# Optimization experiments

Hardware: AMD Instinct MI355X
Metric: run time of the kernel (lower is better)

Reference implementation:

```python
import jax, jax.numpy as jnp
import numpy as np

B, S, D = 4, 2048, 2048  # batch, seq, input_dim == state_dim
N = D

def setup_inputs() -> dict:
    key = jax.random.key(0)
    ks = jax.random.split(key, 6)
    x = jax.random.normal(ks[0], (B, S, D), dtype=jnp.float32)
    W_dt = jax.random.normal(ks[1], (N, D), dtype=jnp.float32) / np.sqrt(D)
    b_dt = jnp.ones((N,), dtype=jnp.float32)  # dt_proj.bias.fill_(1.0)
    W_B = jax.random.normal(ks[2], (N, D), dtype=jnp.float32) / np.sqrt(D)
    W_C = jax.random.normal(ks[3], (D, N), dtype=jnp.float32) / np.sqrt(N)
    A_log = jax.random.normal(ks[4], (N,), dtype=jnp.float32) * 0.5 - 1.0
    D_skip = jnp.zeros((D,), dtype=jnp.float32)
    return {"x": x, "W_dt": W_dt, "b_dt": b_dt, "W_B": W_B, "W_C": W_C,
            "A_log": A_log, "D_skip": D_skip}

def reference(x, W_dt, b_dt, W_B, W_C, A_log, D_skip):
    # dt = softplus(x @ W_dt^T + b_dt) -> [B,S,N]
    dt = jax.nn.softplus(jnp.einsum('bsd,nd->bsn', x, W_dt) + b_dt)
    Bp = jnp.einsum('bsd,nd->bsn', x, W_B)          # [B,S,N]
    A = -jnp.exp(A_log)                              # [N]
    A_bar = jnp.exp(dt * A)                          # [B,S,N]
    inputs = (dt * Bp) * x                           # B_bar * x (N == D)
    # selective scan: h_t = A_bar_t * h_{t-1} + inputs_t
    h0 = jnp.zeros((x.shape[0], A_log.shape[0]), dtype=x.dtype)
    def step(h, ab_u):
        ab, u = ab_u
        h = ab * h + u
        return h, h
    # scan over time axis: move S to leading axis
    _, h_all = jax.lax.scan(step, h0,
                            (jnp.swapaxes(A_bar, 0, 1), jnp.swapaxes(inputs, 0, 1)))
    h_all = jnp.swapaxes(h_all, 0, 1)                # [B,S,N]
    out = jnp.einsum('bsn,dn->bsd', h_all, W_C) + D_skip * x
    return out
```

## Files before the change

### kernel.cpp

```cpp
#include <hip/hip_runtime.h>

#define SEQ    2048
#define DIM    2048
#define NBATCH 4
#define MTOT   (NBATCH * SEQ)
#define CHUNKS 32
#define CLEN   (SEQ / CHUNKS)
#define HT_ELEMS (256 * 32)

typedef __bf16 bf16_t;
typedef __bf16 bf16x8 __attribute__((ext_vector_type(8)));
typedef float  f32x4  __attribute__((ext_vector_type(4)));
typedef unsigned short u16x4 __attribute__((ext_vector_type(4)));
typedef unsigned short u16x2 __attribute__((ext_vector_type(2)));

typedef __attribute__((address_space(3))) bf16_t lds_bf16;

__device__ __forceinline__ unsigned short f2bf_rne(float f) {
    unsigned int u = __float_as_uint(f);
    u += 0x7fffu + ((u >> 16) & 1u);
    return (unsigned short)(u >> 16);
}
__device__ __forceinline__ float bf2f(unsigned short v) {
    return __uint_as_float((unsigned int)v << 16);
}

__global__ void k_convert(const float* __restrict__ src,
                          unsigned short* __restrict__ dst, int n4) {
    int i = blockIdx.x * blockDim.x + threadIdx.x;
    if (i >= n4) return;
    f32x4 v = ((const f32x4*)src)[i];
    u16x4 o;
    o[0] = f2bf_rne(v[0]); o[1] = f2bf_rne(v[1]);
    o[2] = f2bf_rne(v[2]); o[3] = f2bf_rne(v[3]);
    ((u16x4*)dst)[i] = o;
}

__global__ void k_convert_ilv(const float* __restrict__ src,
                              unsigned short* __restrict__ dst, int n4, int phase) {
    int i = blockIdx.x * blockDim.x + threadIdx.x;
    if (i >= n4) return;
    const int R4 = DIM / 4;
    int nrow = i / R4;
    int dcol = i - nrow * R4;
    f32x4 v = ((const f32x4*)src)[i];
    u16x4 o;
    o[0] = f2bf_rne(v[0]); o[1] = f2bf_rne(v[1]);
    o[2] = f2bf_rne(v[2]); o[3] = f2bf_rne(v[3]);
    ((u16x4*)dst)[(2 * nrow + phase) * R4 + dcol] = o;
}

__global__ void k_prep_a(const float* __restrict__ A_log, float* __restrict__ negA, int n) {
    int i = blockIdx.x * blockDim.x + threadIdx.x;
    if (i < n) negA[i] = -__expf(A_log[i]);
}

__device__ __forceinline__ void stage_half(const bf16_t* __restrict__ g, long rowbase,
                                           int K, int k0, bf16_t* lds,
                                           int wave, int lane) {
    const int rl     = lane >> 2;
    const int gchunk = (lane & 3) ^ ((lane >> 3) & 3);
#pragma unroll
    for (int q = 0; q < 2; q++) {
        const bf16_t* ga = g + (rowbase + wave * 32 + q * 16 + rl) * (long)K
                             + k0 + gchunk * 8;
        __builtin_amdgcn_global_load_lds(
            (const __attribute__((address_space(1))) void*)ga,
            (__attribute__((address_space(3))) void*)((char*)lds + (wave * 32 + q * 16) * 64),
            16, 0, 0);
    }
}

#define MFMA_B16(a, b, c) __builtin_amdgcn_mfma_f32_16x16x32_bf16(a, b, c, 0, 0, 0)
#define BAR  __builtin_amdgcn_s_barrier()
#define SBAR __builtin_amdgcn_sched_barrier(0)
#define DSR(D, P) asm volatile("ds_read_b128 %0, %1" : "=v"(D) : "v"(P))

template <int KTILES>
__device__ __forceinline__ void gemm256_main(const bf16_t* __restrict__ A,
                                             const bf16_t* __restrict__ Bm,
                                             int K, long arow0, long brow0,
                                             bf16_t* As, bf16_t* Bs,
                                             f32x4 acc[8][4],
                                             int wave, int lane, int wm, int wn) {
    const int l15  = lane & 15;
    const int quad = lane >> 4;
    const int swz  = (quad ^ ((l15 >> 1) & 3)) * 8;
    const int aoff = (wm * 128 + l15) * 32 + swz;
    const int boff = (wn * 64  + l15) * 32 + swz;

    const lds_bf16* Aw = ((const lds_bf16*)As) + aoff;
    const lds_bf16* Bw = ((const lds_bf16*)Bs) + boff;

    auto stA = [&](int buf, int ks, int kt) {
        stage_half(A, arow0, K, kt * 64 + ks * 32, As + (buf * 2 + ks) * HT_ELEMS, wave, lane);
    };
    auto stB = [&](int buf, int ks, int kt) {
        stage_half(Bm, brow0, K, kt * 64 + ks * 32, Bs + (buf * 2 + ks) * HT_ELEMS, wave, lane);
    };

    stB(0, 0, 0); stA(0, 0, 0); stB(0, 1, 0); stA(0, 1, 0);
    stB(1, 0, 1); stA(1, 0, 1); stB(1, 1, 1);
    asm volatile("s_waitcnt vmcnt(6)");
    SBAR;
    BAR;

    bf16x8 a0, a1, a2, a3, b0, b1, b2, b3;

#define LDA03(BUF, KS) { const lds_bf16* p = Aw + ((BUF) * 2 + (KS)) * HT_ELEMS; \
    DSR(a0, p); DSR(a1, p + 512); DSR(a2, p + 1024); DSR(a3, p + 1536); }
#define LDA47(BUF, KS) { const lds_bf16* p = Aw + ((BUF) * 2 + (KS)) * HT_ELEMS + 2048; \
    DSR(a0, p); DSR(a1, p + 512); DSR(a2, p + 1024); DSR(a3, p + 1536); }
#define LDB(BUF, KS)  { const lds_bf16* p = Bw + ((BUF) * 2 + (KS)) * HT_ELEMS; \
    DSR(b0, p); DSR(b1, p + 512); DSR(b2, p + 1024); DSR(b3, p + 1536); }
#define MM16(I0) \
    SBAR; \
    BAR; \
    asm volatile("s_waitcnt lgkmcnt(0)"); \
    SBAR; \
    __builtin_amdgcn_s_setprio(1); \
    acc[(I0)+0][0] = MFMA_B16(a0, b0, acc[(I0)+0][0]); \
    acc[(I0)+0][1] = MFMA_B16(a0, b1, acc[(I0)+0][1]); \
    acc[(I0)+0][2] = MFMA_B16(a0, b2, acc[(I0)+0][2]); \
    acc[(I0)+0][3] = MFMA_B16(a0, b3, acc[(I0)+0][3]); \
    acc[(I0)+1][0] = MFMA_B16(a1, b0, acc[(I0)+1][0]); \
    acc[(I0)+1][1] = MFMA_B16(a1, b1, acc[(I0)+1][1]); \
    acc[(I0)+1][2] = MFMA_B16(a1, b2, acc[(I0)+1][2]); \
    acc[(I0)+1][3] = MFMA_B16(a1, b3, acc[(I0)+1][3]); \
    acc[(I0)+2][0] = MFMA_B16(a2, b0, acc[(I0)+2][0]); \
    acc[(I0)+2][1] = MFMA_B16(a2, b1, acc[(I0)+2][1]); \
    acc[(I0)+2][2] = MFMA_B16(a2, b2, acc[(I0)+2][2]); \
    acc[(I0)+2][3] = MFMA_B16(a2, b3, acc[(I0)+2][3]); \
    acc[(I0)+3][0] = MFMA_B16(a3, b0, acc[(I0)+3][0]); \
    acc[(I0)+3][1] = MFMA_B16(a3, b1, acc[(I0)+3][1]); \
    acc[(I0)+3][2] = MFMA_B16(a3, b2, acc[(I0)+3][2]); \
    acc[(I0)+3][3] = MFMA_B16(a3, b3, acc[(I0)+3][3]); \
    __builtin_amdgcn_s_setprio(0); \
    SBAR; \
    BAR;

#pragma unroll 1
    for (int t = 0; t < KTILES / 2; ++t) {
        const bool nlast = (t != KTILES / 2 - 1);
        const int k1 = 2 * t + 1, k2 = 2 * t + 2, k3 = 2 * t + 3;
        LDA03(0, 0); LDB(0, 0);
        stA(1, 1, k1);
        MM16(0);
        LDA47(0, 0);
        if (nlast) stB(0, 0, k2);
        MM16(4);
        LDA03(0, 1); LDB(0, 1);
        if (nlast) stA(0, 0, k2);
        MM16(0);
        LDA47(0, 1);
        if (nlast) stB(0, 1, k2);
        if (nlast) { asm volatile("s_waitcnt vmcnt(6)"); }
        else       { asm volatile("s_waitcnt vmcnt(0)"); }
        MM16(4);
        LDA03(1, 0); LDB(1, 0);
        if (nlast) stA(0, 1, k2);
        MM16(0);
        LDA47(1, 0);
        if (nlast) stB(1, 0, k3);
        MM16(4);
        LDA03(1, 1); LDB(1, 1);
        if (nlast) stA(1, 0, k3);
        MM16(0);
        LDA47(1, 1);
        if (nlast) stB(1, 1, k3);
        if (nlast) { asm volatile("s_waitcnt vmcnt(6)"); }
        MM16(4);
    }
#undef LDA03
#undef LDA47
#undef LDB
#undef MM16
}

__global__ __launch_bounds__(512, 2)
void k_gemm_fused(const bf16_t* __restrict__ A, const bf16_t* __restrict__ Wcat,
                  const float* __restrict__ x, const float* __restrict__ b_dt,
                  const float* __restrict__ negA,
                  unsigned short* __restrict__ abuf, unsigned short* __restrict__ ubuf) {
    __shared__ __align__(16) bf16_t As[4 * HT_ELEMS];
    __shared__ __align__(16) bf16_t Bs[4 * HT_ELEMS];

    const int tid  = threadIdx.x;
    const int lane = tid & 63;
    const int wave = tid >> 6;
    const int wm   = wave >> 2;
    const int wn   = wave & 3;
    int flat = blockIdx.x;
    int swzb = (flat & 7) * 64 + (flat >> 3);
    int bm = swzb & 31;
    int bn = swzb >> 5;

    f32x4 acc[8][4];
#pragma unroll
    for (int i = 0; i < 8; i++)
#pragma unroll
        for (int j = 0; j < 4; j++) acc[i][j] = (f32x4){0.f, 0.f, 0.f, 0.f};

    gemm256_main<DIM / 64>(A, Wcat, DIM, (long)bm * 256, (long)bn * 256,
                           As, Bs, acc, wave, lane, wm, wn);

    const int l15  = lane & 15;
    const int quad = lane >> 4;
    const int odd  = l15 & 1;
#pragma unroll
    for (int i = 0; i < 8; i++) {
#pragma unroll
        for (int j = 0; j < 4; j++) {
#pragma unroll
            for (int r = 0; r < 4; r++) {
                float v = acc[i][j][r];
                float w = __shfl_xor(v, 1);
                float dtpre = odd ? w : v;
                float bpv   = odd ? v : w;
                long row = (long)bm * 256 + wm * 128 + i * 16 + quad * 4 + r;
                int  col = bn * 256 + wn * 64 + j * 16 + l15;
                int  n   = col >> 1;
                float z  = dtpre + b_dt[n];
                float dt = (z > 15.f) ? z : __logf(1.f + __expf(z));
                float a  = __expf(negA[n] * dt);
                float u  = dt * bpv * x[row * DIM + n];
                long idx = row * DIM + n;
                if (odd) ubuf[idx] = f2bf_rne(u); else abuf[idx] = f2bf_rne(a);
            }
        }
    }
}

__global__ __launch_bounds__(512, 2)
void k_gemm_bt(const bf16_t* __restrict__ A, const bf16_t* __restrict__ Bm,
               float* __restrict__ C, int N, int K,
               const float* __restrict__ skip, const float* __restrict__ xres) {
    __shared__ __align__(16) bf16_t As[4 * HT_ELEMS];
    __shared__ __align__(16) bf16_t Bs[4 * HT_ELEMS];

    const int tid  = threadIdx.x;
    const int lane = tid & 63;
    const int wave = tid >> 6;
    const int wm   = wave >> 2;
    const int wn   = wave & 3;
    int flat = blockIdx.x;
    int swzb = (flat & 7) * 32 + (flat >> 3);
    int bm = swzb & 31;
    int bn = swzb >> 5;

    f32x4 acc[8][4];
#pragma unroll
    for (int i = 0; i < 8; i++)
#pragma unroll
        for (int j = 0; j < 4; j++) acc[i][j] = (f32x4){0.f, 0.f, 0.f, 0.f};

    gemm256_main<DIM / 64>(A, Bm, K, (long)bm * 256, (long)bn * 256,
                           As, Bs, acc, wave, lane, wm, wn);

    const int l15  = lane & 15;
    const int quad = lane >> 4;
#pragma unroll
    for (int i = 0; i < 8; i++) {
#pragma unroll
        for (int j = 0; j < 4; j++) {
#pragma unroll
            for (int r = 0; r < 4; r++) {
                long row = (long)bm * 256 + wm * 128 + i * 16 + quad * 4 + r;
                long col = (long)bn * 256 + wn * 64 + j * 16 + l15;
                long idx = row * (long)N + col;
                float v = acc[i][j][r];
                if (skip) v += skip[col] * xres[idx];
                C[idx] = v;
            }
        }
    }
}

__global__ void k_scan1(const unsigned short* __restrict__ a,
                        const unsigned short* __restrict__ u,
                        float* __restrict__ P, float* __restrict__ V) {
    int t  = blockIdx.x * blockDim.x + threadIdx.x;
    int n2 = t & (DIM / 2 - 1);
    int c  = (t >> 10) & (CHUNKS - 1);
    int b  = t >> 15;
    long base = ((long)b * SEQ + (long)c * CLEN) * DIM + n2 * 2;
    float p0 = 1.f, v0 = 0.f, p1 = 1.f, v1 = 0.f;
    for (int s = 0; s < CLEN; s++) {
        u16x2 av = *(const u16x2*)(a + base + (long)s * DIM);
        u16x2 uv = *(const u16x2*)(u + base + (long)s * DIM);
        float a0 = bf2f(av[0]), a1 = bf2f(av[1]);
        v0 = a0 * v0 + bf2f(uv[0]);  p0 *= a0;
        v1 = a1 * v1 + bf2f(uv[1]);  p1 *= a1;
    }
    long pidx = ((long)b * CHUNKS + c) * DIM + n2 * 2;
    *(float2*)(P + pidx) = make_float2(p0, p1);
    *(float2*)(V + pidx) = make_float2(v0, v1);
}

__global__ void k_scan2(const float* __restrict__ P, const float* __restrict__ V,
                        float* __restrict__ carry) {
    int t = blockIdx.x * blockDim.x + threadIdx.x;
    int n = t & (DIM - 1);
    int b = t >> 11;
    float H = 0.f;
    for (int c = 0; c < CHUNKS; c++) {
        long idx = ((long)b * CHUNKS + c) * DIM + n;
        carry[idx] = H;
        H = P[idx] * H + V[idx];
    }
}

__global__ void k_scan3(const unsigned short* __restrict__ a,
                        const unsigned short* __restrict__ u,
                        const float* __restrict__ carry,
                        unsigned short* __restrict__ h) {
    int t  = blockIdx.x * blockDim.x + threadIdx.x;
    int n2 = t & (DIM / 2 - 1);
    int c  = (t >> 10) & (CHUNKS - 1);
    int b  = t >> 15;
    long base = ((long)b * SEQ + (long)c * CLEN) * DIM + n2 * 2;
    long cidx = ((long)b * CHUNKS + c) * DIM + n2 * 2;
    float2 Hc = *(const float2*)(carry + cidx);
    float H0 = Hc.x, H1 = Hc.y;
    for (int s = 0; s < CLEN; s++) {
        u16x2 av = *(const u16x2*)(a + base + (long)s * DIM);
        u16x2 uv = *(const u16x2*)(u + base + (long)s * DIM);
        H0 = bf2f(av[0]) * H0 + bf2f(uv[0]);
        H1 = bf2f(av[1]) * H1 + bf2f(uv[1]);
        u16x2 o; o[0] = f2bf_rne(H0); o[1] = f2bf_rne(H1);
        *(u16x2*)(h + base + (long)s * DIM) = o;
    }
}

extern "C" void kernel_launch(void* const* d_in, const int* in_sizes, int n_in,
                              void* d_out, int out_size, void* d_ws, size_t ws_size,
                              hipStream_t stream) {
    const float* x      = (const float*)d_in[0];
    const float* W_dt   = (const float*)d_in[1];
    const float* b_dt   = (const float*)d_in[2];
    const float* W_B    = (const float*)d_in[3];
    const float* W_C    = (const float*)d_in[4];
    const float* A_log  = (const float*)d_in[5];
    const float* D_skip = (const float*)d_in[6];
    float* out = (float*)d_out;

    char* ws = (char*)d_ws;
    size_t off = 0;
    auto alloc = [&](size_t bytes) -> char* {
        char* p = ws + off;
        off += (bytes + 255) & ~(size_t)255;
        return p;
    };
    unsigned short* xb   = (unsigned short*)alloc((size_t)MTOT * DIM * 2);
    unsigned short* wcat = (unsigned short*)alloc((size_t)2 * DIM * DIM * 2);
    unsigned short* wcb  = (unsigned short*)alloc((size_t)DIM * DIM * 2);
    unsigned short* abuf = (unsigned short*)alloc((size_t)MTOT * DIM * 2);
    unsigned short* ubuf = (unsigned short*)alloc((size_t)MTOT * DIM * 2);
    float* P     = (float*)alloc((size_t)NBATCH * CHUNKS * DIM * 4);
    float* V     = (float*)alloc((size_t)NBATCH * CHUNKS * DIM * 4);
    float* carry = (float*)alloc((size_t)NBATCH * CHUNKS * DIM * 4);
    float* negA  = (float*)alloc((size_t)DIM * 4);

    const int n4x = MTOT * DIM / 4;
    const int n4w = DIM * DIM / 4;
    k_convert<<<n4x / 256, 256, 0, stream>>>(x, xb, n4x);
    k_convert_ilv<<<n4w / 256, 256, 0, stream>>>(W_dt, wcat, n4w, 0);
    k_convert_ilv<<<n4w / 256, 256, 0, stream>>>(W_B,  wcat, n4w, 1);
    k_convert<<<n4w / 256, 256, 0, stream>>>(W_C, wcb, n4w);
    k_prep_a<<<DIM / 256, 256, 0, stream>>>(A_log, negA, DIM);

    k_gemm_fused<<<(MTOT / 256) * (2 * DIM / 256), 512, 0, stream>>>(
        (const bf16_t*)xb, (const bf16_t*)wcat, x, b_dt, negA, abuf, ubuf);

    const int scan2_threads = NBATCH * CHUNKS * DIM / 2;
    k_scan1<<<scan2_threads / 256, 256, 0, stream>>>(abuf, ubuf, P, V);
    k_scan2<<<(NBATCH * DIM) / 256, 256, 0, stream>>>(P, V, carry);
    k_scan3<<<scan2_threads / 256, 256, 0, stream>>>(abuf, ubuf, carry, xb );

    k_gemm_bt<<<(MTOT / 256) * (DIM / 256), 512, 0, stream>>>(
        (const bf16_t*)xb, (const bf16_t*)wcb, out, DIM, DIM, D_skip, x);
}
```

Before: 501.0 us.

## Use partial LDS waits in GEMM inner loop and raise scan chunk count

The GEMM inner loop now interleaves the A and B LDS reads and swaps the single full lgkmcnt(0) wait for staged partial waits, reordering the MFMAs so each one starts as soon as its operands arrive. This is meant to overlap LDS read latency with matrix-core work. Separately, the chunked scan goes from 32 to 128 chunks, giving scan1 and scan3 four times as many threads with shorter sequential loops for more parallelism. The cost is a longer serial loop in scan2 and larger P/V/carry buffers.

```diff
diff --git a/kernel.cpp b/kernel.cpp
--- a/kernel.cpp
+++ b/kernel.cpp
@@ -4,8 +4,9 @@
 #define DIM    2048
 #define NBATCH 4
 #define MTOT   (NBATCH * SEQ)
-#define CHUNKS 32
+#define CHUNKS 128
 #define CLEN   (SEQ / CHUNKS)
+#define CSH    7
 #define HT_ELEMS (256 * 32)
 
 typedef __bf16 bf16_t;
@@ -75,6 +76,8 @@
 #define BAR  __builtin_amdgcn_s_barrier()
 #define SBAR __builtin_amdgcn_sched_barrier(0)
 #define DSR(D, P) asm volatile("ds_read_b128 %0, %1" : "=v"(D) : "v"(P))
+#define WAITL(N) do { asm volatile("s_waitcnt lgkmcnt(" #N ")"); \
+                      __builtin_amdgcn_sched_barrier(0); } while (0)
 
 template <int KTILES>
 __device__ __forceinline__ void gemm256_main(const bf16_t* __restrict__ A,
@@ -107,74 +110,105 @@
 
     bf16x8 a0, a1, a2, a3, b0, b1, b2, b3;
 
-#define LDA03(BUF, KS) { const lds_bf16* p = Aw + ((BUF) * 2 + (KS)) * HT_ELEMS; \
-    DSR(a0, p); DSR(a1, p + 512); DSR(a2, p + 1024); DSR(a3, p + 1536); }
-#define LDA47(BUF, KS) { const lds_bf16* p = Aw + ((BUF) * 2 + (KS)) * HT_ELEMS + 2048; \
-    DSR(a0, p); DSR(a1, p + 512); DSR(a2, p + 1024); DSR(a3, p + 1536); }
-#define LDB(BUF, KS)  { const lds_bf16* p = Bw + ((BUF) * 2 + (KS)) * HT_ELEMS; \
-    DSR(b0, p); DSR(b1, p + 512); DSR(b2, p + 1024); DSR(b3, p + 1536); }
-#define MM16(I0) \
-    SBAR; \
-    BAR; \
-    asm volatile("s_waitcnt lgkmcnt(0)"); \
-    SBAR; \
+#define LDAB03(BUF, KS) { \
+    const lds_bf16* pa = Aw + ((BUF) * 2 + (KS)) * HT_ELEMS; \
+    const lds_bf16* pb = Bw + ((BUF) * 2 + (KS)) * HT_ELEMS; \
+    DSR(a0, pa);        DSR(b0, pb); \
+    DSR(a1, pa + 512);  DSR(b1, pb + 512); \
+    DSR(a2, pa + 1024); DSR(b2, pb + 1024); \
+    DSR(a3, pa + 1536); DSR(b3, pb + 1536); }
+#define LDA47(BUF, KS) { \
+    const lds_bf16* pa = Aw + ((BUF) * 2 + (KS)) * HT_ELEMS + 2048; \
+    DSR(a0, pa); DSR(a1, pa + 512); DSR(a2, pa + 1024); DSR(a3, pa + 1536); }
+
+#define MM16A(I0) \
+    SBAR; BAR; \
+    WAITL(6); \
     __builtin_amdgcn_s_setprio(1); \
     acc[(I0)+0][0] = MFMA_B16(a0, b0, acc[(I0)+0][0]); \
+    WAITL(4); \
     acc[(I0)+0][1] = MFMA_B16(a0, b1, acc[(I0)+0][1]); \
-    acc[(I0)+0][2] = MFMA_B16(a0, b2, acc[(I0)+0][2]); \
-    acc[(I0)+0][3] = MFMA_B16(a0, b3, acc[(I0)+0][3]); \
     acc[(I0)+1][0] = MFMA_B16(a1, b0, acc[(I0)+1][0]); \
     acc[(I0)+1][1] = MFMA_B16(a1, b1, acc[(I0)+1][1]); \
+    WAITL(2); \
+    acc[(I0)+0][2] = MFMA_B16(a0, b2, acc[(I0)+0][2]); \
     acc[(I0)+1][2] = MFMA_B16(a1, b2, acc[(I0)+1][2]); \
-    acc[(I0)+1][3] = MFMA_B16(a1, b3, acc[(I0)+1][3]); \
     acc[(I0)+2][0] = MFMA_B16(a2, b0, acc[(I0)+2][0]); \
     acc[(I0)+2][1] = MFMA_B16(a2, b1, acc[(I0)+2][1]); \
     acc[(I0)+2][2] = MFMA_B16(a2, b2, acc[(I0)+2][2]); \
+    WAITL(0); \
+    acc[(I0)+0][3] = MFMA_B16(a0, b3, acc[(I0)+0][3]); \
+    acc[(I0)+1][3] = MFMA_B16(a1, b3, acc[(I0)+1][3]); \
     acc[(I0)+2][3] = MFMA_B16(a2, b3, acc[(I0)+2][3]); \
     acc[(I0)+3][0] = MFMA_B16(a3, b0, acc[(I0)+3][0]); \
     acc[(I0)+3][1] = MFMA_B16(a3, b1, acc[(I0)+3][1]); \
     acc[(I0)+3][2] = MFMA_B16(a3, b2, acc[(I0)+3][2]); \
     acc[(I0)+3][3] = MFMA_B16(a3, b3, acc[(I0)+3][3]); \
     __builtin_amdgcn_s_setprio(0); \
-    SBAR; \
-    BAR;
+    SBAR; BAR;
+
+#define MM16B(I0) \
+    SBAR; BAR; \
+    WAITL(3); \
+    __builtin_amdgcn_s_setprio(1); \
+    acc[(I0)+0][0] = MFMA_B16(a0, b0, acc[(I0)+0][0]); \
+    acc[(I0)+0][1] = MFMA_B16(a0, b1, acc[(I0)+0][1]); \
+    acc[(I0)+0][2] = MFMA_B16(a0, b2, acc[(I0)+0][2]); \
+    acc[(I0)+0][3] = MFMA_B16(a0, b3, acc[(I0)+0][3]); \
+    WAITL(2); \
+    acc[(I0)+1][0] = MFMA_B16(a1, b0, acc[(I0)+1][0]); \
+    acc[(I0)+1][1] = MFMA_B16(a1, b1, acc[(I0)+1][1]); \
+    acc[(I0)+1][2] = MFMA_B16(a1, b2, acc[(I0)+1][2]); \
+    acc[(I0)+1][3] = MFMA_B16(a1, b3, acc[(I0)+1][3]); \
+    WAITL(1); \
+    acc[(I0)+2][0] = MFMA_B16(a2, b0, acc[(I0)+2][0]); \
+    acc[(I0)+2][1] = MFMA_B16(a2, b1, acc[(I0)+2][1]); \
+    acc[(I0)+2][2] = MFMA_B16(a2, b2, acc[(I0)+2][2]); \
+    acc[(I0)+2][3] = MFMA_B16(a2, b3, acc[(I0)+2][3]); \
+    WAITL(0); \
+    acc[(I0)+3][0] = MFMA_B16(a3, b0, acc[(I0)+3][0]); \
+    acc[(I0)+3][1] = MFMA_B16(a3, b1, acc[(I0)+3][1]); \
+    acc[(I0)+3][2] = MFMA_B16(a3, b2, acc[(I0)+3][2]); \
+    acc[(I0)+3][3] = MFMA_B16(a3, b3, acc[(I0)+3][3]); \
+    __builtin_amdgcn_s_setprio(0); \
+    SBAR; BAR;
 
 #pragma unroll 1
     for (int t = 0; t < KTILES / 2; ++t) {
         const bool nlast = (t != KTILES / 2 - 1);
         const int k1 = 2 * t + 1, k2 = 2 * t + 2, k3 = 2 * t + 3;
-        LDA03(0, 0); LDB(0, 0);
+        LDAB03(0, 0);
         stA(1, 1, k1);
-        MM16(0);
+        MM16A(0);
         LDA47(0, 0);
         if (nlast) stB(0, 0, k2);
-        MM16(4);
-        LDA03(0, 1); LDB(0, 1);
+        MM16B(4);
+        LDAB03(0, 1);
         if (nlast) stA(0, 0, k2);
-        MM16(0);
+        MM16A(0);
         LDA47(0, 1);
         if (nlast) stB(0, 1, k2);
         if (nlast) { asm volatile("s_waitcnt vmcnt(6)"); }
         else       { asm volatile("s_waitcnt vmcnt(0)"); }
-        MM16(4);
-        LDA03(1, 0); LDB(1, 0);
+        MM16B(4);
+        LDAB03(1, 0);
         if (nlast) stA(0, 1, k2);
-        MM16(0);
+        MM16A(0);
         LDA47(1, 0);
         if (nlast) stB(1, 0, k3);
-        MM16(4);
-        LDA03(1, 1); LDB(1, 1);
+        MM16B(4);
+        LDAB03(1, 1);
         if (nlast) stA(1, 0, k3);
-        MM16(0);
+        MM16A(0);
         LDA47(1, 1);
         if (nlast) stB(1, 1, k3);
         if (nlast) { asm volatile("s_waitcnt vmcnt(6)"); }
-        MM16(4);
-    }
-#undef LDA03
+        MM16B(4);
+    }
+#undef LDAB03
 #undef LDA47
-#undef LDB
-#undef MM16
+#undef MM16A
+#undef MM16B
 }
 
 __global__ __launch_bounds__(512, 2)
@@ -282,7 +316,7 @@
     int t  = blockIdx.x * blockDim.x + threadIdx.x;
     int n2 = t & (DIM / 2 - 1);
     int c  = (t >> 10) & (CHUNKS - 1);
-    int b  = t >> 15;
+    int b  = t >> (10 + CSH);
     long base = ((long)b * SEQ + (long)c * CLEN) * DIM + n2 * 2;
     float p0 = 1.f, v0 = 0.f, p1 = 1.f, v1 = 0.f;
     for (int s = 0; s < CLEN; s++) {
@@ -317,7 +351,7 @@
     int t  = blockIdx.x * blockDim.x + threadIdx.x;
     int n2 = t & (DIM / 2 - 1);
     int c  = (t >> 10) & (CHUNKS - 1);
-    int b  = t >> 15;
+    int b  = t >> (10 + CSH);
     long base = ((long)b * SEQ + (long)c * CLEN) * DIM + n2 * 2;
     long cidx = ((long)b * CHUNKS + c) * DIM + n2 * 2;
     float2 Hc = *(const float2*)(carry + cidx);
@@ -372,10 +406,10 @@
     k_gemm_fused<<<(MTOT / 256) * (2 * DIM / 256), 512, 0, stream>>>(
         (const bf16_t*)xb, (const bf16_t*)wcat, x, b_dt, negA, abuf, ubuf);
 
-    const int scan2_threads = NBATCH * CHUNKS * DIM / 2;
-    k_scan1<<<scan2_threads / 256, 256, 0, stream>>>(abuf, ubuf, P, V);
+    const int scan_threads = NBATCH * CHUNKS * DIM / 2;
+    k_scan1<<<scan_threads / 256, 256, 0, stream>>>(abuf, ubuf, P, V);
     k_scan2<<<(NBATCH * DIM) / 256, 256, 0, stream>>>(P, V, carry);
-    k_scan3<<<scan2_threads / 256, 256, 0, stream>>>(abuf, ubuf, carry, xb );
+    k_scan3<<<scan_threads / 256, 256, 0, stream>>>(abuf, ubuf, carry, xb );
 
     k_gemm_bt<<<(MTOT / 256) * (DIM / 256), 512, 0, stream>>>(
         (const bf16_t*)xb, (const bf16_t*)wcb, out, DIM, DIM, D_skip, x);
```

Measured after the change: 509.9 us. Within noise of the previous version (+1.8%).

## Double-buffer LDS fragment registers to overlap ds_reads with MFMA phases

Applied to the files above, without the earlier changes.

Restructures the GEMM main loop so the LDS fragments for the next MFMA phase are read into a second register set while the current phase's MFMAs run. Each phase now has a single barrier instead of two. The prologue stages all eight tile halves, and vmcnt waits are adjusted to allow eight loads in flight. This costs more VGPRs for the extra fragment registers, which could pressure occupancy under launch_bounds(512,2). The CSH macro in the scan kernels is a cosmetic rename with the same shift value.

```diff
diff --git a/kernel.cpp b/kernel.cpp
--- a/kernel.cpp
+++ b/kernel.cpp
@@ -6,6 +6,7 @@
 #define MTOT   (NBATCH * SEQ)
 #define CHUNKS 32
 #define CLEN   (SEQ / CHUNKS)
+#define CSH    5
 #define HT_ELEMS (256 * 32)
 
 typedef __bf16 bf16_t;
@@ -75,6 +76,10 @@
 #define BAR  __builtin_amdgcn_s_barrier()
 #define SBAR __builtin_amdgcn_sched_barrier(0)
 #define DSR(D, P) asm volatile("ds_read_b128 %0, %1" : "=v"(D) : "v"(P))
+#define PRIO1 __builtin_amdgcn_s_setprio(1)
+#define PRIO0 __builtin_amdgcn_s_setprio(0)
+#define WAIT0 do { asm volatile("s_waitcnt lgkmcnt(0)"); SBAR; } while (0)
+#define ENDPH do { SBAR; BAR; } while (0)
 
 template <int KTILES>
 __device__ __forceinline__ void gemm256_main(const bf16_t* __restrict__ A,
@@ -99,81 +104,111 @@
         stage_half(Bm, brow0, K, kt * 64 + ks * 32, Bs + (buf * 2 + ks) * HT_ELEMS, wave, lane);
     };
 
+    bf16x8 aA0, aA1, aA2, aA3, aB0, aB1, aB2, aB3;
+    bf16x8 b00, b01, b02, b03, b10, b11, b12, b13;
+
+#define RD_FULL(BUF, KS, A0, A1, A2, A3, B0, B1, B2, B3) { \
+    const lds_bf16* pa = Aw + ((BUF) * 2 + (KS)) * HT_ELEMS; \
+    const lds_bf16* pb = Bw + ((BUF) * 2 + (KS)) * HT_ELEMS; \
+    DSR(A0, pa);        DSR(B0, pb); \
+    DSR(A1, pa + 512);  DSR(B1, pb + 512); \
+    DSR(A2, pa + 1024); DSR(B2, pb + 1024); \
+    DSR(A3, pa + 1536); DSR(B3, pb + 1536); }
+#define RD_HALF(BUF, KS, A0, A1, A2, A3) { \
+    const lds_bf16* pa = Aw + ((BUF) * 2 + (KS)) * HT_ELEMS + 2048; \
+    DSR(A0, pa); DSR(A1, pa + 512); DSR(A2, pa + 1024); DSR(A3, pa + 1536); }
+#define MM16(I0, A0, A1, A2, A3, B0, B1, B2, B3) do { \
+    PRIO1; \
+    acc[(I0)+0][0] = MFMA_B16(A0, B0, acc[(I0)+0][0]); \
+    acc[(I0)+0][1] = MFMA_B16(A0, B1, acc[(I0)+0][1]); \
+    acc[(I0)+0][2] = MFMA_B16(A0, B2, acc[(I0)+0][2]); \
+    acc[(I0)+0][3] = MFMA_B16(A0, B3, acc[(I0)+0][3]); \
+    acc[(I0)+1][0] = MFMA_B16(A1, B0, acc[(I0)+1][0]); \
+    acc[(I0)+1][1] = MFMA_B16(A1, B1, acc[(I0)+1][1]); \
+    acc[(I0)+1][2] = MFMA_B16(A1, B2, acc[(I0)+1][2]); \
+    acc[(I0)+1][3] = MFMA_B16(A1, B3, acc[(I0)+1][3]); \
+    acc[(I0)+2][0] = MFMA_B16(A2, B0, acc[(I0)+2][0]); \
+    acc[(I0)+2][1] = MFMA_B16(A2, B1, acc[(I0)+2][1]); \
+    acc[(I0)+2][2] = MFMA_B16(A2, B2, acc[(I0)+2][2]); \
+    acc[(I0)+2][3] = MFMA_B16(A2, B3, acc[(I0)+2][3]); \
+    acc[(I0)+3][0] = MFMA_B16(A3, B0, acc[(I0)+3][0]); \
+    acc[(I0)+3][1] = MFMA_B16(A3, B1, acc[(I0)+3][1]); \
+    acc[(I0)+3][2] = MFMA_B16(A3, B2, acc[(I0)+3][2]); \
+    acc[(I0)+3][3] = MFMA_B16(A3, B3, acc[(I0)+3][3]); \
+    PRIO0; } while (0)
+
     stB(0, 0, 0); stA(0, 0, 0); stB(0, 1, 0); stA(0, 1, 0);
-    stB(1, 0, 1); stA(1, 0, 1); stB(1, 1, 1);
-    asm volatile("s_waitcnt vmcnt(6)");
+    stB(1, 0, 1); stA(1, 0, 1); stB(1, 1, 1); stA(1, 1, 1);
+    asm volatile("s_waitcnt vmcnt(0)");
     SBAR;
     BAR;
-
-    bf16x8 a0, a1, a2, a3, b0, b1, b2, b3;
-
-#define LDA03(BUF, KS) { const lds_bf16* p = Aw + ((BUF) * 2 + (KS)) * HT_ELEMS; \
-    DSR(a0, p); DSR(a1, p + 512); DSR(a2, p + 1024); DSR(a3, p + 1536); }
-#define LDA47(BUF, KS) { const lds_bf16* p = Aw + ((BUF) * 2 + (KS)) * HT_ELEMS + 2048; \
-    DSR(a0, p); DSR(a1, p + 512); DSR(a2, p + 1024); DSR(a3, p + 1536); }
-#define LDB(BUF, KS)  { const lds_bf16* p = Bw + ((BUF) * 2 + (KS)) * HT_ELEMS; \
-    DSR(b0, p); DSR(b1, p + 512); DSR(b2, p + 1024); DSR(b3, p + 1536); }
-#define MM16(I0) \
-    SBAR; \
-    BAR; \
-    asm volatile("s_waitcnt lgkmcnt(0)"); \
-    SBAR; \
-    __builtin_amdgcn_s_setprio(1); \
-    acc[(I0)+0][0] = MFMA_B16(a0, b0, acc[(I0)+0][0]); \
-    acc[(I0)+0][1] = MFMA_B16(a0, b1, acc[(I0)+0][1]); \
-    acc[(I0)+0][2] = MFMA_B16(a0, b2, acc[(I0)+0][2]); \
-    acc[(I0)+0][3] = MFMA_B16(a0, b3, acc[(I0)+0][3]); \
-    acc[(I0)+1][0] = MFMA_B16(a1, b0, acc[(I0)+1][0]); \
-    acc[(I0)+1][1] = MFMA_B16(a1, b1, acc[(I0)+1][1]); \
-    acc[(I0)+1][2] = MFMA_B16(a1, b2, acc[(I0)+1][2]); \
-    acc[(I0)+1][3] = MFMA_B16(a1, b3, acc[(I0)+1][3]); \
-    acc[(I0)+2][0] = MFMA_B16(a2, b0, acc[(I0)+2][0]); \
-    acc[(I0)+2][1] = MFMA_B16(a2, b1, acc[(I0)+2][1]); \
-    acc[(I0)+2][2] = MFMA_B16(a2, b2, acc[(I0)+2][2]); \
-    acc[(I0)+2][3] = MFMA_B16(a2, b3, acc[(I0)+2][3]); \
-    acc[(I0)+3][0] = MFMA_B16(a3, b0, acc[(I0)+3][0]); \
-    acc[(I0)+3][1] = MFMA_B16(a3, b1, acc[(I0)+3][1]); \
-    acc[(I0)+3][2] = MFMA_B16(a3, b2, acc[(I0)+3][2]); \
-    acc[(I0)+3][3] = MFMA_B16(a3, b3, acc[(I0)+3][3]); \
-    __builtin_amdgcn_s_setprio(0); \
-    SBAR; \
-    BAR;
+    RD_FULL(0, 0, aA0, aA1, aA2, aA3, b00, b01, b02, b03);
 
 #pragma unroll 1
     for (int t = 0; t < KTILES / 2; ++t) {
         const bool nlast = (t != KTILES / 2 - 1);
         const int k1 = 2 * t + 1, k2 = 2 * t + 2, k3 = 2 * t + 3;
-        LDA03(0, 0); LDB(0, 0);
-        stA(1, 1, k1);
-        MM16(0);
-        LDA47(0, 0);
+
+        WAIT0;
+        RD_HALF(0, 0, aB0, aB1, aB2, aB3);
+        if (t) stA(1, 1, k1);
+        SBAR; asm volatile("s_waitcnt vmcnt(8)"); SBAR;
+        MM16(0, aA0, aA1, aA2, aA3, b00, b01, b02, b03);
+        ENDPH;
+        WAIT0;
+        RD_FULL(0, 1, aA0, aA1, aA2, aA3, b10, b11, b12, b13);
         if (nlast) stB(0, 0, k2);
-        MM16(4);
-        LDA03(0, 1); LDB(0, 1);
+        SBAR;
+        MM16(4, aB0, aB1, aB2, aB3, b00, b01, b02, b03);
+        ENDPH;
+        WAIT0;
+        RD_HALF(0, 1, aB0, aB1, aB2, aB3);
         if (nlast) stA(0, 0, k2);
-        MM16(0);
-        LDA47(0, 1);
+        SBAR;
+        if (nlast) { asm volatile("s_waitcnt vmcnt(8)"); }
+        else       { asm volatile("s_waitcnt vmcnt(4)"); }
+        SBAR;
+        MM16(0, aA0, aA1, aA2, aA3, b10, b11, b12, b13);
+        ENDPH;
+        WAIT0;
+        RD_FULL(1, 0, aA0, aA1, aA2, aA3, b00, b01, b02, b03);
         if (nlast) stB(0, 1, k2);
-        if (nlast) { asm volatile("s_waitcnt vmcnt(6)"); }
+        SBAR;
+        MM16(4, aB0, aB1, aB2, aB3, b10, b11, b12, b13);
+        ENDPH;
+        WAIT0;
+        RD_HALF(1, 0, aB0, aB1, aB2, aB3);
+        if (nlast) stA(0, 1, k2);
+        SBAR;
+        if (nlast) { asm volatile("s_waitcnt vmcnt(8)"); }
         else       { asm volatile("s_waitcnt vmcnt(0)"); }
-        MM16(4);
-        LDA03(1, 0); LDB(1, 0);
-        if (nlast) stA(0, 1, k2);
-        MM16(0);
-        LDA47(1, 0);
+        SBAR;
+        MM16(0, aA0, aA1, aA2, aA3, b00, b01, b02, b03);
+        ENDPH;
+        WAIT0;
+        RD_FULL(1, 1, aA0, aA1, aA2, aA3, b10, b11, b12, b13);
         if (nlast) stB(1, 0, k3);
-        MM16(4);
-        LDA03(1, 1); LDB(1, 1);
+        SBAR;
+        MM16(4, aB0, aB1, aB2, aB3, b00, b01, b02, b03);
+        ENDPH;
+        WAIT0;
+        RD_HALF(1, 1, aB0, aB1, aB2, aB3);
         if (nlast) stA(1, 0, k3);
-        MM16(0);
-        LDA47(1, 1);
-        if (nlast) stB(1, 1, k3);
-        if (nlast) { asm volatile("s_waitcnt vmcnt(6)"); }
-        MM16(4);
-    }
-#undef LDA03
-#undef LDA47
-#undef LDB
+        SBAR;
+        if (nlast) { asm volatile("s_waitcnt vmcnt(8)"); SBAR; }
+        MM16(0, aA0, aA1, aA2, aA3, b10, b11, b12, b13);
+        ENDPH;
+        WAIT0;
+        if (nlast) {
+            RD_FULL(0, 0, aA0, aA1, aA2, aA3, b00, b01, b02, b03);
+            stB(1, 1, k3);
+        }
+        SBAR;
+        MM16(4, aB0, aB1, aB2, aB3, b10, b11, b12, b13);
+        ENDPH;
+    }
+#undef RD_FULL
+#undef RD_HALF
 #undef MM16
 }
 
@@ -282,7 +317,7 @@
     int t  = blockIdx.x * blockDim.x + threadIdx.x;
     int n2 = t & (DIM / 2 - 1);
     int c  = (t >> 10) & (CHUNKS - 1);
-    int b  = t >> 15;
+    int b  = t >> (10 + CSH);
     long base = ((long)b * SEQ + (long)c * CLEN) * DIM + n2 * 2;
     float p0 = 1.f, v0 = 0.f, p1 = 1.f, v1 = 0.f;
     for (int s = 0; s < CLEN; s++) {
@@ -317,7 +352,7 @@
     int t  = blockIdx.x * blockDim.x + threadIdx.x;
     int n2 = t & (DIM / 2 - 1);
     int c  = (t >> 10) & (CHUNKS - 1);
-    int b  = t >> 15;
+    int b  = t >> (10 + CSH);
     long base = ((long)b * SEQ + (long)c * CLEN) * DIM + n2 * 2;
     long cidx = ((long)b * CHUNKS + c) * DIM + n2 * 2;
     float2 Hc = *(const float2*)(carry + cidx);
@@ -372,10 +407,10 @@
     k_gemm_fused<<<(MTOT / 256) * (2 * DIM / 256), 512, 0, stream>>>(
         (const bf16_t*)xb, (const bf16_t*)wcat, x, b_dt, negA, abuf, ubuf);
 
-    const int scan2_threads = NBATCH * CHUNKS * DIM / 2;
-    k_scan1<<<scan2_threads / 256, 256, 0, stream>>>(abuf, ubuf, P, V);
+    const int scan_threads = NBATCH * CHUNKS * DIM / 2;
+    k_scan1<<<scan_threads / 256, 256, 0, stream>>>(abuf, ubuf, P, V);
     k_scan2<<<(NBATCH * DIM) / 256, 256, 0, stream>>>(P, V, carry);
-    k_scan3<<<scan2_threads / 256, 256, 0, stream>>>(abuf, ubuf, carry, xb );
+    k_scan3<<<scan_threads / 256, 256, 0, stream>>>(abuf, ubuf, carry, xb );
 
     k_gemm_bt<<<(MTOT / 256) * (DIM / 256), 512, 0, stream>>>(
         (const bf16_t*)xb, (const bf16_t*)wcb, out, DIM, DIM, D_skip, x);
```

New measurement: 536.7 us. +7.1%, slower.
